# Kernel tuning notes

Measured on AMD Instinct MI355X. Metric: run time of the kernel, lower is better.

Reference implementation:

```python
import jax, jax.numpy as jnp
import numpy as np

DIM = 1024
NUM_HEADS = 16
HEAD_DIM = DIM // NUM_HEADS
SCALE = HEAD_DIM ** -0.5


def setup_inputs() -> dict:
    key = jax.random.key(0)
    k1, k2, k3, k4 = jax.random.split(key, 4)
    B, N = 2, 2048
    x = jax.random.normal(k1, (B, N, DIM), dtype=jnp.float32)
    # qkv: Linear(dim, 3*dim, bias=False); torch stores weight as [out, in]
    W_qkv = jax.random.normal(k2, (3 * DIM, DIM), dtype=jnp.float32) * (DIM ** -0.5)
    # proj: Linear(dim, dim, bias=True)
    W_proj = jax.random.normal(k3, (DIM, DIM), dtype=jnp.float32) * (DIM ** -0.5)
    b_proj = jax.random.normal(k4, (DIM,), dtype=jnp.float32) * 0.01
    return {"x": x, "W_qkv": W_qkv, "W_proj": W_proj, "b_proj": b_proj}


def reference(x, W_qkv, W_proj, b_proj):
    B, N, C = x.shape
    H, D = NUM_HEADS, HEAD_DIM
    # qkv projection: [B,N,3C] -> [3,B,H,N,D]
    qkv = jnp.einsum('bnc,oc->bno', x, W_qkv)
    qkv = qkv.reshape(B, N, 3, H, D).transpose(2, 0, 3, 1, 4)
    q, k, v = qkv[0] * SCALE, qkv[1], qkv[2]
    # full attention matrix [B,H,N,N] (faithful to manual impl)
    attn = jnp.einsum('bhqd,bhkd->bhqk', q, k)
    attn = jax.nn.softmax(attn, axis=-1)
    # dropout p=0.0 -> identity (eval semantics)
    out = jnp.einsum('bhqk,bhkd->bhqd', attn, v)  # [B,H,N,D]
    out = out.transpose(0, 2, 1, 3).reshape(B, N, C)
    out = jnp.einsum('bnc,oc->bno', out, W_proj) + b_proj
    return out
```

## Files before the change

kernel.cpp:

```cpp
#include <hip/hip_runtime.h>
#include <math.h>

#define BATCH 2
#define NTOK  2048
#define DIMC  1024
#define NH    16
#define HD    64
#define SOFT_K2 0.18033688011112042f

typedef __bf16 bf16;
typedef __attribute__((ext_vector_type(8))) __bf16 bf16x8;
typedef __attribute__((ext_vector_type(4))) __bf16 bf16x4;
typedef __attribute__((ext_vector_type(4))) float f32x4;

__device__ __forceinline__ void load_lds16(const void* g, void* l) {
    __builtin_amdgcn_global_load_lds(
        (const __attribute__((address_space(1))) void*)g,
        (__attribute__((address_space(3))) void*)l, 16, 0, 0);
}
__device__ __forceinline__ f32x4 mfma16(bf16x8 a, bf16x8 b, f32x4 c) {
    return __builtin_amdgcn_mfma_f32_16x16x32_bf16(a, b, c, 0, 0, 0);
}

__global__ __launch_bounds__(256) void cast3(
    const float* __restrict__ x,  const float* __restrict__ w1, const float* __restrict__ w2,
    bf16* __restrict__ xb, bf16* __restrict__ w1b, bf16* __restrict__ w2b)
{
    int blk = blockIdx.x;
    const float* src; bf16* dst; size_t base;
    if (blk < 4096)      { src = x;  dst = xb;  base = (size_t)blk * 1024; }
    else if (blk < 7168) { src = w1; dst = w1b; base = (size_t)(blk - 4096) * 1024; }
    else                 { src = w2; dst = w2b; base = (size_t)(blk - 7168) * 1024; }
    size_t i = base + (size_t)threadIdx.x * 4;
    float4 v = *(const float4*)(src + i);
    bf16x4 r;
    r[0] = (bf16)v.x; r[1] = (bf16)v.y; r[2] = (bf16)v.z; r[3] = (bf16)v.w;
    *(bf16x4*)(dst + i) = r;
}

__global__ __launch_bounds__(256) void gemm_qkv(
    const bf16* __restrict__ A, const bf16* __restrict__ B,
    bf16* __restrict__ Cq, bf16* __restrict__ vt,
    int M, int N, int K)
{
    __shared__ __align__(16) bf16 smem[17408];

    const int tid  = threadIdx.x;
    const int w    = tid >> 6, lane = tid & 63;
    const int wm   = w & 1,  wn = w >> 1;
    const int m0   = blockIdx.y * 128, n0 = blockIdx.x * 128;
    const int lm   = lane & 15, quad = lane >> 4;

    const bf16* Ag[2]; const bf16* Bg[2];
#pragma unroll
    for (int t = 0; t < 2; ++t) {
        int c = t * 256 + tid;
        Ag[t] = A + (size_t)(m0 + (c & 127)) * K + (c >> 7) * 8;
        Bg[t] = B + (size_t)(n0 + (c & 127)) * K + (c >> 7) * 8;
    }

    f32x4 acc[4][4];
    f32x4 z4 = {0.f, 0.f, 0.f, 0.f};
#pragma unroll
    for (int i = 0; i < 4; ++i)
#pragma unroll
        for (int j = 0; j < 4; ++j) acc[i][j] = z4;

#define QKV_STAGE(kt, b_) do {                                                  \
    for (int t = 0; t < 2; ++t) {                                               \
        load_lds16(Ag[t] + (kt), smem + (b_) * 4096 + (t * 256 + w * 64) * 8);  \
        load_lds16(Bg[t] + (kt), smem + 8192 + (b_) * 4096 + (t * 256 + w * 64) * 8); \
    } } while (0)

    const int NI = K / 32;
    QKV_STAGE(0, 0);
    __syncthreads();
    for (int it = 0; it < NI; ++it) {
        const int buf = it & 1;
        if (it + 1 < NI) QKV_STAGE((it + 1) * 32, buf ^ 1);
        const bf16* Asb = smem + buf * 4096;
        const bf16* Bsb = smem + 8192 + buf * 4096;
        bf16x8 af[4], bf_[4];
#pragma unroll
        for (int mi = 0; mi < 4; ++mi)
            af[mi] = *(const bf16x8*)(Asb + (quad * 128 + wm * 64 + mi * 16 + lm) * 8);
#pragma unroll
        for (int ni = 0; ni < 4; ++ni)
            bf_[ni] = *(const bf16x8*)(Bsb + (quad * 128 + wn * 64 + ni * 16 + lm) * 8);
#pragma unroll
        for (int mi = 0; mi < 4; ++mi)
#pragma unroll
            for (int ni = 0; ni < 4; ++ni)
                acc[mi][ni] = mfma16(af[mi], bf_[ni], acc[mi][ni]);
        __syncthreads();
    }
#undef QKV_STAGE

    if (n0 >= 2048) {
        bf16* T = smem;
#pragma unroll
        for (int ni = 0; ni < 4; ++ni) {
            const int dl = wn * 64 + ni * 16 + lm;
#pragma unroll
            for (int mi = 0; mi < 4; ++mi)
#pragma unroll
                for (int r = 0; r < 4; ++r)
                    T[dl * 136 + wm * 64 + mi * 16 + quad * 4 + r] = (bf16)acc[mi][ni][r];
        }
        __syncthreads();
        const int gcol0 = n0 - 2048;
        const int bb = m0 >> 11, tokbase = m0 & 2047;
#pragma unroll
        for (int rep = 0; rep < 8; ++rep) {
            const int g = rep * 256 + tid;
            const int d = g >> 4, tc = g & 15;
            bf16x8 v = *(const bf16x8*)&T[d * 136 + tc * 8];
            const int gcol = gcol0 + d, hh = gcol >> 6, dd = gcol & 63;
            *(bf16x8*)(vt + ((size_t)((bb * NH + hh) * HD + dd)) * NTOK + tokbase + tc * 8) = v;
        }
    } else {
#pragma unroll
        for (int ni = 0; ni < 4; ++ni) {
            const int col = n0 + wn * 64 + ni * 16 + lm;
#pragma unroll
            for (int mi = 0; mi < 4; ++mi)
#pragma unroll
                for (int r = 0; r < 4; ++r) {
                    const int row = m0 + wm * 64 + mi * 16 + quad * 4 + r;
                    Cq[(size_t)row * N + col] = (bf16)acc[mi][ni][r];
                }
        }
    }
}

__global__ __launch_bounds__(256) void gemm_proj(
    const bf16* __restrict__ A, const bf16* __restrict__ B,
    const float* __restrict__ bias, float* __restrict__ C,
    int M, int N, int K)
{
    __shared__ __align__(16) bf16 smem[12288];

    const int tid  = threadIdx.x;
    const int w    = tid >> 6, lane = tid & 63;
    const int wm   = w & 1,  wn = w >> 1;
    const int m0   = blockIdx.y * 64, n0 = blockIdx.x * 128;
    const int lm   = lane & 15, quad = lane >> 4;

    const bf16* Ag = A + (size_t)(m0 + (tid & 63)) * K + (tid >> 6) * 8;
    const bf16* Bg[2];
#pragma unroll
    for (int t = 0; t < 2; ++t) {
        int c = t * 256 + tid;
        Bg[t] = B + (size_t)(n0 + (c & 127)) * K + (c >> 7) * 8;
    }

    f32x4 acc[2][4];
    f32x4 z4 = {0.f, 0.f, 0.f, 0.f};
#pragma unroll
    for (int i = 0; i < 2; ++i)
#pragma unroll
        for (int j = 0; j < 4; ++j) acc[i][j] = z4;

#define PROJ_STAGE(kt, b_) do {                                                 \
    load_lds16(Ag + (kt), smem + (b_) * 2048 + (w * 64) * 8);                   \
    for (int t = 0; t < 2; ++t)                                                 \
        load_lds16(Bg[t] + (kt), smem + 4096 + (b_) * 4096 + (t * 256 + w * 64) * 8); \
    } while (0)

    const int NI = K / 32;
    PROJ_STAGE(0, 0);
    __syncthreads();
    for (int it = 0; it < NI; ++it) {
        const int buf = it & 1;
        if (it + 1 < NI) PROJ_STAGE((it + 1) * 32, buf ^ 1);
        const bf16* Asb = smem + buf * 2048;
        const bf16* Bsb = smem + 4096 + buf * 4096;
        bf16x8 af[2], bf_[4];
#pragma unroll
        for (int mi = 0; mi < 2; ++mi)
            af[mi] = *(const bf16x8*)(Asb + (quad * 64 + wm * 32 + mi * 16 + lm) * 8);
#pragma unroll
        for (int ni = 0; ni < 4; ++ni)
            bf_[ni] = *(const bf16x8*)(Bsb + (quad * 128 + wn * 64 + ni * 16 + lm) * 8);
#pragma unroll
        for (int mi = 0; mi < 2; ++mi)
#pragma unroll
            for (int ni = 0; ni < 4; ++ni)
                acc[mi][ni] = mfma16(af[mi], bf_[ni], acc[mi][ni]);
        __syncthreads();
    }
#undef PROJ_STAGE

#pragma unroll
    for (int ni = 0; ni < 4; ++ni) {
        const int col = n0 + wn * 64 + ni * 16 + lm;
        const float bi = bias[col];
#pragma unroll
        for (int mi = 0; mi < 2; ++mi)
#pragma unroll
            for (int r = 0; r < 4; ++r) {
                const int row = m0 + wm * 32 + mi * 16 + quad * 4 + r;
                C[(size_t)row * N + col] = acc[mi][ni][r] + bi;
            }
    }
}

__global__ __launch_bounds__(256, 2) void attn_mfma(
    const bf16* __restrict__ qkv,
    const bf16* __restrict__ Vt,
    bf16* __restrict__ att)
{
    __shared__ __align__(16) bf16 Ks[2][64 * 64];
    __shared__ __align__(16) bf16 Vs[2][64 * 64];
    __shared__ __align__(16) bf16 Ps[2][128 * 72];

    const int n0 = blockIdx.x * 128, h = blockIdx.y, b = blockIdx.z;
    const int tid = threadIdx.x, w = tid >> 6, lane = tid & 63;
    const int lm = lane & 15, quad = lane >> 4;

    const size_t rs = (size_t)(3 * DIMC);
    const bf16* qbase  = qkv + (size_t)b * NTOK * rs + h * HD;
    const bf16* kbase  = qbase + DIMC;
    const bf16* vtbase = Vt + ((size_t)(b * NH + h) * HD) * NTOK;

    bf16x8 aq[2][2];
#pragma unroll
    for (int g = 0; g < 2; ++g)
#pragma unroll
        for (int s2 = 0; s2 < 2; ++s2)
            aq[g][s2] = *(const bf16x8*)(qbase
                + (size_t)(n0 + w * 32 + g * 16 + lm) * rs + s2 * 32 + quad * 8);

    const int l0 = (w * 2 + 0) * 64 + lane, l1 = (w * 2 + 1) * 64 + lane;
    const bf16* kg0 = kbase + (size_t)(l0 & 63) * rs + (l0 >> 6) * 8;
    const bf16* kg1 = kbase + (size_t)(l1 & 63) * rs + (l1 >> 6) * 8;
    const bf16* vg0 = vtbase + (size_t)(l0 & 63) * NTOK + (l0 >> 6) * 8;
    const bf16* vg1 = vtbase + (size_t)(l1 & 63) * NTOK + (l1 >> 6) * 8;

#define STAGE_K(tile, dst) do { \
    load_lds16(kg0 + (size_t)(tile) * 64 * rs, (dst) + (w * 2 + 0) * 512); \
    load_lds16(kg1 + (size_t)(tile) * 64 * rs, (dst) + (w * 2 + 1) * 512); } while (0)
#define STAGE_V(tile, dst) do { \
    load_lds16(vg0 + (size_t)(tile) * 64, (dst) + (w * 2 + 0) * 512); \
    load_lds16(vg1 + (size_t)(tile) * 64, (dst) + (w * 2 + 1) * 512); } while (0)

    f32x4 O[2][4];
    f32x4 z4 = {0.f, 0.f, 0.f, 0.f};
#pragma unroll
    for (int g = 0; g < 2; ++g)
#pragma unroll
        for (int ni = 0; ni < 4; ++ni) O[g][ni] = z4;
    float lsum[2][4] = {{0.f, 0.f, 0.f, 0.f}, {0.f, 0.f, 0.f, 0.f}};

#define COMPUTE_S_PS(Ksb, Psb) do {                                           \
    f32x4 S[2][4];                                                            \
    for (int g = 0; g < 2; ++g)                                               \
        for (int ni = 0; ni < 4; ++ni) S[g][ni] = z4;                         \
    for (int s2 = 0; s2 < 2; ++s2)                                            \
        for (int ni = 0; ni < 4; ++ni) {                                      \
            bf16x8 bk = *(const bf16x8*)((Ksb)                                \
                + ((s2 * 4 + quad) * 64 + ni * 16 + lm) * 8);                 \
            S[0][ni] = mfma16(aq[0][s2], bk, S[0][ni]);                       \
            S[1][ni] = mfma16(aq[1][s2], bk, S[1][ni]);                       \
        }                                                                     \
    for (int g = 0; g < 2; ++g)                                               \
        for (int ni = 0; ni < 4; ++ni)                                        \
            for (int r = 0; r < 4; ++r) {                                     \
                const float p = __builtin_amdgcn_exp2f(S[g][ni][r] * SOFT_K2);\
                (Psb)[(w * 32 + g * 16 + quad * 4 + r) * 72 + ni * 16 + lm]   \
                    = (bf16)p;                                                \
                lsum[g][r] += p;                                              \
            }                                                                 \
} while (0)

#define COMPUTE_PV(Psb, Vsb) do {                                             \
    for (int s2 = 0; s2 < 2; ++s2) {                                          \
        bf16x8 ap0 = *(const bf16x8*)((Psb)                                   \
            + (w * 32 + lm) * 72 + s2 * 32 + quad * 8);                       \
        bf16x8 ap1 = *(const bf16x8*)((Psb)                                   \
            + (w * 32 + 16 + lm) * 72 + s2 * 32 + quad * 8);                  \
        for (int ni = 0; ni < 4; ++ni) {                                      \
            bf16x8 bv = *(const bf16x8*)((Vsb)                                \
                + ((s2 * 4 + quad) * 64 + ni * 16 + lm) * 8);                 \
            O[0][ni] = mfma16(ap0, bv, O[0][ni]);                             \
            O[1][ni] = mfma16(ap1, bv, O[1][ni]);                             \
        }                                                                     \
    }                                                                         \
} while (0)

    const int NT = NTOK / 64;

    STAGE_K(0, Ks[0]);
    STAGE_V(0, Vs[0]);
    STAGE_K(1, Ks[1]);
    __syncthreads();
    COMPUTE_S_PS(Ks[0], Ps[0]);

    for (int t = 0; t < NT; ++t) {
        __syncthreads();
        if (t + 2 < NT) STAGE_K(t + 2, Ks[t & 1]);
        if (t + 1 < NT) STAGE_V(t + 1, Vs[(t + 1) & 1]);
        if (t + 1 < NT) COMPUTE_S_PS(Ks[(t + 1) & 1], Ps[(t + 1) & 1]);
        COMPUTE_PV(Ps[t & 1], Vs[t & 1]);
    }

#undef STAGE_K
#undef STAGE_V
#undef COMPUTE_S_PS
#undef COMPUTE_PV

#pragma unroll
    for (int g = 0; g < 2; ++g)
#pragma unroll
        for (int r = 0; r < 4; ++r) {
#pragma unroll
            for (int msk = 1; msk < 16; msk <<= 1)
                lsum[g][r] += __shfl_xor(lsum[g][r], msk);
        }

#pragma unroll
    for (int g = 0; g < 2; ++g)
#pragma unroll
        for (int r = 0; r < 4; ++r) {
            const float invl = 1.0f / lsum[g][r];
            const size_t row = (size_t)(b * NTOK + n0 + w * 32 + g * 16 + quad * 4 + r);
#pragma unroll
            for (int ni = 0; ni < 4; ++ni)
                att[row * DIMC + h * HD + ni * 16 + lm] = (bf16)(O[g][ni][r] * invl);
        }
}

extern "C" void kernel_launch(void* const* d_in, const int* in_sizes, int n_in,
                              void* d_out, int out_size, void* d_ws, size_t ws_size,
                              hipStream_t stream)
{
    const float* x      = (const float*)d_in[0];
    const float* W_qkv  = (const float*)d_in[1];
    const float* W_proj = (const float*)d_in[2];
    const float* b_proj = (const float*)d_in[3];
    float* out = (float*)d_out;

    char* ws = (char*)d_ws;
    bf16* xb   = (bf16*)ws;
    bf16* w1b  = (bf16*)(ws + (8u  << 20));
    bf16* w2b  = (bf16*)(ws + (14u << 20));
    bf16* qkvb = (bf16*)(ws + (16u << 20));
    bf16* vt   = (bf16*)(ws + (40u << 20));
    bf16* attb = (bf16*)(ws + (48u << 20));

    const int M = BATCH * NTOK;

    cast3<<<8192, 256, 0, stream>>>(x, W_qkv, W_proj, xb, w1b, w2b);

    gemm_qkv<<<dim3((3 * DIMC) / 128, M / 128), 256, 0, stream>>>(
        xb, w1b, qkvb, vt, M, 3 * DIMC, DIMC);

    attn_mfma<<<dim3(NTOK / 128, NH, BATCH), 256, 0, stream>>>(qkvb, vt, attb);

    gemm_proj<<<dim3(DIMC / 128, M / 64), 256, 0, stream>>>(
        attb, w2b, b_proj, out, M, DIMC, DIMC);
}
```

Measured before the change: 239.1 us.

## Stage GEMM tiles through registers with single LDS buffer and BK=64

Both projection GEMMs drop the double-buffered direct global-to-LDS loads. They now prefetch the next K tile into registers during compute, then write it to a single LDS buffer between two barriers. The K step doubles from 32 to 64, halving loop iterations and barriers per tile, and launch bounds now ask for 3 blocks per CU. This adds register pressure and a second barrier per iteration, and the LDS writes are no longer overlapped with compute.

```diff
diff --git a/kernel.cpp b/kernel.cpp
--- a/kernel.cpp
+++ b/kernel.cpp
@@ -38,7 +38,8 @@
     *(bf16x4*)(dst + i) = r;
 }
 
-__global__ __launch_bounds__(256) void gemm_qkv(
+
+__global__ __launch_bounds__(256, 3) void gemm_qkv(
     const bf16* __restrict__ A, const bf16* __restrict__ B,
     bf16* __restrict__ Cq, bf16* __restrict__ vt,
     int M, int N, int K)
@@ -51,13 +52,20 @@
     const int m0   = blockIdx.y * 128, n0 = blockIdx.x * 128;
     const int lm   = lane & 15, quad = lane >> 4;
 
-    const bf16* Ag[2]; const bf16* Bg[2];
-#pragma unroll
-    for (int t = 0; t < 2; ++t) {
-        int c = t * 256 + tid;
-        Ag[t] = A + (size_t)(m0 + (c & 127)) * K + (c >> 7) * 8;
-        Bg[t] = B + (size_t)(n0 + (c & 127)) * K + (c >> 7) * 8;
-    }
+    const bf16* Arow = A + (size_t)(m0 + (tid & 127)) * K + (tid >> 7) * 8;
+    const bf16* Brow = B + (size_t)(n0 + (tid & 127)) * K + (tid >> 7) * 8;
+
+    bf16x8 ar[4], br[4];
+#define QKV_LOADREG(kt) do {                                    \
+    for (int t = 0; t < 4; ++t) {                               \
+        ar[t] = *(const bf16x8*)(Arow + (kt) + t * 16);         \
+        br[t] = *(const bf16x8*)(Brow + (kt) + t * 16);         \
+    } } while (0)
+#define QKV_DSWRITE() do {                                      \
+    for (int t = 0; t < 4; ++t) {                               \
+        *(bf16x8*)(smem + (t * 256 + tid) * 8) = ar[t];         \
+        *(bf16x8*)(smem + 8192 + (t * 256 + tid) * 8) = br[t];  \
+    } } while (0)
 
     f32x4 acc[4][4];
     f32x4 z4 = {0.f, 0.f, 0.f, 0.f};
@@ -66,35 +74,35 @@
 #pragma unroll
         for (int j = 0; j < 4; ++j) acc[i][j] = z4;
 
-#define QKV_STAGE(kt, b_) do {                                                  \
-    for (int t = 0; t < 2; ++t) {                                               \
-        load_lds16(Ag[t] + (kt), smem + (b_) * 4096 + (t * 256 + w * 64) * 8);  \
-        load_lds16(Bg[t] + (kt), smem + 8192 + (b_) * 4096 + (t * 256 + w * 64) * 8); \
-    } } while (0)
-
-    const int NI = K / 32;
-    QKV_STAGE(0, 0);
+    const int NI = K / 64;
+    QKV_LOADREG(0);
+    QKV_DSWRITE();
     __syncthreads();
     for (int it = 0; it < NI; ++it) {
-        const int buf = it & 1;
-        if (it + 1 < NI) QKV_STAGE((it + 1) * 32, buf ^ 1);
-        const bf16* Asb = smem + buf * 4096;
-        const bf16* Bsb = smem + 8192 + buf * 4096;
-        bf16x8 af[4], bf_[4];
-#pragma unroll
-        for (int mi = 0; mi < 4; ++mi)
-            af[mi] = *(const bf16x8*)(Asb + (quad * 128 + wm * 64 + mi * 16 + lm) * 8);
-#pragma unroll
-        for (int ni = 0; ni < 4; ++ni)
-            bf_[ni] = *(const bf16x8*)(Bsb + (quad * 128 + wn * 64 + ni * 16 + lm) * 8);
-#pragma unroll
-        for (int mi = 0; mi < 4; ++mi)
+        if (it + 1 < NI) QKV_LOADREG((it + 1) * 64);
+#pragma unroll
+        for (int s = 0; s < 2; ++s) {
+            bf16x8 af[4], bf_[4];
+#pragma unroll
+            for (int mi = 0; mi < 4; ++mi)
+                af[mi] = *(const bf16x8*)(smem
+                    + ((s * 4 + quad) * 128 + wm * 64 + mi * 16 + lm) * 8);
 #pragma unroll
             for (int ni = 0; ni < 4; ++ni)
-                acc[mi][ni] = mfma16(af[mi], bf_[ni], acc[mi][ni]);
-        __syncthreads();
-    }
-#undef QKV_STAGE
+                bf_[ni] = *(const bf16x8*)(smem + 8192
+                    + ((s * 4 + quad) * 128 + wn * 64 + ni * 16 + lm) * 8);
+#pragma unroll
+            for (int mi = 0; mi < 4; ++mi)
+#pragma unroll
+                for (int ni = 0; ni < 4; ++ni)
+                    acc[mi][ni] = mfma16(af[mi], bf_[ni], acc[mi][ni]);
+        }
+        __syncthreads();
+        if (it + 1 < NI) QKV_DSWRITE();
+        __syncthreads();
+    }
+#undef QKV_LOADREG
+#undef QKV_DSWRITE
 
     if (n0 >= 2048) {
         bf16* T = smem;
@@ -133,7 +141,7 @@
     }
 }
 
-__global__ __launch_bounds__(256) void gemm_proj(
+__global__ __launch_bounds__(256, 3) void gemm_proj(
     const bf16* __restrict__ A, const bf16* __restrict__ B,
     const float* __restrict__ bias, float* __restrict__ C,
     int M, int N, int K)
@@ -146,13 +154,22 @@
     const int m0   = blockIdx.y * 64, n0 = blockIdx.x * 128;
     const int lm   = lane & 15, quad = lane >> 4;
 
-    const bf16* Ag = A + (size_t)(m0 + (tid & 63)) * K + (tid >> 6) * 8;
-    const bf16* Bg[2];
-#pragma unroll
-    for (int t = 0; t < 2; ++t) {
-        int c = t * 256 + tid;
-        Bg[t] = B + (size_t)(n0 + (c & 127)) * K + (c >> 7) * 8;
-    }
+    const bf16* Arow = A + (size_t)(m0 + (tid & 63)) * K + (tid >> 6) * 8;
+    const bf16* Brow = B + (size_t)(n0 + (tid & 127)) * K + (tid >> 7) * 8;
+
+    bf16x8 ar[2], br[4];
+#define PROJ_LOADREG(kt) do {                                   \
+    for (int t = 0; t < 2; ++t)                                 \
+        ar[t] = *(const bf16x8*)(Arow + (kt) + t * 32);         \
+    for (int t = 0; t < 4; ++t)                                 \
+        br[t] = *(const bf16x8*)(Brow + (kt) + t * 16);         \
+    } while (0)
+#define PROJ_DSWRITE() do {                                     \
+    for (int t = 0; t < 2; ++t)                                 \
+        *(bf16x8*)(smem + (t * 256 + tid) * 8) = ar[t];         \
+    for (int t = 0; t < 4; ++t)                                 \
+        *(bf16x8*)(smem + 4096 + (t * 256 + tid) * 8) = br[t];  \
+    } while (0)
 
     f32x4 acc[2][4];
     f32x4 z4 = {0.f, 0.f, 0.f, 0.f};
@@ -161,35 +178,35 @@
 #pragma unroll
         for (int j = 0; j < 4; ++j) acc[i][j] = z4;
 
-#define PROJ_STAGE(kt, b_) do {                                                 \
-    load_lds16(Ag + (kt), smem + (b_) * 2048 + (w * 64) * 8);                   \
-    for (int t = 0; t < 2; ++t)                                                 \
-        load_lds16(Bg[t] + (kt), smem + 4096 + (b_) * 4096 + (t * 256 + w * 64) * 8); \
-    } while (0)
-
-    const int NI = K / 32;
-    PROJ_STAGE(0, 0);
+    const int NI = K / 64;
+    PROJ_LOADREG(0);
+    PROJ_DSWRITE();
     __syncthreads();
     for (int it = 0; it < NI; ++it) {
-        const int buf = it & 1;
-        if (it + 1 < NI) PROJ_STAGE((it + 1) * 32, buf ^ 1);
-        const bf16* Asb = smem + buf * 2048;
-        const bf16* Bsb = smem + 4096 + buf * 4096;
-        bf16x8 af[2], bf_[4];
-#pragma unroll
-        for (int mi = 0; mi < 2; ++mi)
-            af[mi] = *(const bf16x8*)(Asb + (quad * 64 + wm * 32 + mi * 16 + lm) * 8);
-#pragma unroll
-        for (int ni = 0; ni < 4; ++ni)
-            bf_[ni] = *(const bf16x8*)(Bsb + (quad * 128 + wn * 64 + ni * 16 + lm) * 8);
-#pragma unroll
-        for (int mi = 0; mi < 2; ++mi)
+        if (it + 1 < NI) PROJ_LOADREG((it + 1) * 64);
+#pragma unroll
+        for (int s = 0; s < 2; ++s) {
+            bf16x8 af[2], bf_[4];
+#pragma unroll
+            for (int mi = 0; mi < 2; ++mi)
+                af[mi] = *(const bf16x8*)(smem
+                    + ((s * 4 + quad) * 64 + wm * 32 + mi * 16 + lm) * 8);
 #pragma unroll
             for (int ni = 0; ni < 4; ++ni)
-                acc[mi][ni] = mfma16(af[mi], bf_[ni], acc[mi][ni]);
-        __syncthreads();
-    }
-#undef PROJ_STAGE
+                bf_[ni] = *(const bf16x8*)(smem + 4096
+                    + ((s * 4 + quad) * 128 + wn * 64 + ni * 16 + lm) * 8);
+#pragma unroll
+            for (int mi = 0; mi < 2; ++mi)
+#pragma unroll
+                for (int ni = 0; ni < 4; ++ni)
+                    acc[mi][ni] = mfma16(af[mi], bf_[ni], acc[mi][ni]);
+        }
+        __syncthreads();
+        if (it + 1 < NI) PROJ_DSWRITE();
+        __syncthreads();
+    }
+#undef PROJ_LOADREG
+#undef PROJ_DSWRITE
 
 #pragma unroll
     for (int ni = 0; ni < 4; ++ni) {
```

New measurement: 221.2 us. -7.5%, faster.
